# Kernel optimization log

Measured on AMD Instinct MI355X. Metric: run time of the kernel, lower is better.

## Reference

```python
import jax, jax.numpy as jnp
import numpy as np

SLIDING_WINDOW_SIZE = 512  # matches init_kwargs


def setup_inputs() -> dict:
    key = jax.random.key(0)
    kq, kk, kv = jax.random.split(key, 3)
    B, H, L, E = 2, 16, 2048, 128
    q = jax.random.normal(kq, (B, H, L, E), dtype=jnp.float32)
    k = jax.random.normal(kk, (B, H, L, E), dtype=jnp.float32)
    v = jax.random.normal(kv, (B, H, L, E), dtype=jnp.float32)
    return {"q": q, "k": k, "v": v}


def reference(q, k, v):
    # q: (B,H,L,E), k: (B,H,S,E), v: (B,H,S,Ev)
    B, H, L, E = q.shape
    S = k.shape[2]
    scale = jnp.asarray(1.0 / np.sqrt(E), dtype=q.dtype)  # flex_attention default scale
    # Full scores, then score_mod-style masking (faithful to original, which
    # applies -inf after dense score computation without a BlockMask).
    scores = jnp.einsum("bhle,bhse->bhls", q, k) * scale
    q_idx = jnp.arange(L)[:, None]
    k_idx = jnp.arange(S)[None, :]
    # causal: q_idx < k_idx ; window: q_idx - k_idx > window_size
    mask = (q_idx < k_idx) | (q_idx - k_idx > SLIDING_WINDOW_SIZE)
    scores = jnp.where(mask[None, None], -jnp.inf, scores)
    attn = jax.nn.softmax(scores, axis=-1)
    return jnp.einsum("bhls,bhse->bhle", attn, v)
```

## Files before the change

kernel.cpp:

```cpp
#include <hip/hip_runtime.h>


typedef __bf16 bf16_t;
typedef bf16_t bf16x8 __attribute__((ext_vector_type(8)));
typedef float f32x4 __attribute__((ext_vector_type(4)));

union FragU { bf16x8 v; unsigned short s[8]; };

__device__ __forceinline__ unsigned short f2bf(float f) {
    union { float f; unsigned u; } x; x.f = f;
    unsigned u = x.u;
    u += 0x7fffu + ((u >> 16) & 1u);
    return (unsigned short)(u >> 16);
}

constexpr int B_ = 2, H_ = 16, Lq = 2048, E_ = 128, WIN = 512;
constexpr int QT = 64;
constexpr int KT = 32;
constexpr int KSTR = 128;
constexpr int VSTR = 130;
constexpr int PSTR = 40;

#define SCALE_LOG2E 0.1275174364f

extern "C" __global__ __launch_bounds__(256, 2)
void flexattn_kernel(const float* __restrict__ Q,
                     const float* __restrict__ K,
                     const float* __restrict__ V,
                     float* __restrict__ O)
{
    __shared__ unsigned short sK[KT * KSTR];
    __shared__ unsigned short sV[KT * VSTR];
    __shared__ unsigned short sP[4 * 16 * PSTR];

    const int tid  = threadIdx.x;
    const int w    = tid >> 6;
    const int lane = tid & 63;
    const int c    = lane & 15;
    const int g    = lane >> 4;

    const int q0 = blockIdx.x * QT;
    const int bh = blockIdx.y;
    const size_t base = (size_t)bh * Lq * E_;
    const float* Qp = Q + base;
    const float* Kp = K + base;
    const float* Vp = V + base;
    float*       Op = O + base;

    const int qb = q0 + w * 16;

    FragU qf[4];
    {
        const float* qrow = Qp + (size_t)(qb + c) * E_ + g * 8;
        #pragma unroll
        for (int ck = 0; ck < 4; ++ck) {
            #pragma unroll
            for (int j = 0; j < 8; ++j)
                qf[ck].s[j] = f2bf(qrow[ck * 32 + j] * SCALE_LOG2E);
        }
    }

    f32x4 acc[8];
    #pragma unroll
    for (int n = 0; n < 8; ++n) acc[n] = (f32x4){0.f, 0.f, 0.f, 0.f};
    float m_r[4], l_r[4];
    #pragma unroll
    for (int r = 0; r < 4; ++r) { m_r[r] = -1e30f; l_r[r] = 0.f; }

    const int kv_lo = (q0 - WIN) > 0 ? (q0 - WIN) : 0;
    const int kv_hi = q0 + QT;

    for (int kt = kv_lo; kt < kv_hi; kt += KT) {
        __syncthreads();
        #pragma unroll
        for (int i = 0; i < 4; ++i) {
            int fi  = i * 256 + tid;
            int row = fi >> 5;
            int col = (fi & 31) << 2;
            float4 kx = reinterpret_cast<const float4*>(Kp + (size_t)kt * E_)[fi];
            float4 vx = reinterpret_cast<const float4*>(Vp + (size_t)kt * E_)[fi];
            int kcol = col ^ ((row & 7) * 8);
            ushort4 ku;
            ku.x = f2bf(kx.x); ku.y = f2bf(kx.y); ku.z = f2bf(kx.z); ku.w = f2bf(kx.w);
            *reinterpret_cast<ushort4*>(&sK[row * KSTR + kcol]) = ku;
            ushort2 va, vb;
            va.x = f2bf(vx.x); va.y = f2bf(vx.y);
            vb.x = f2bf(vx.z); vb.y = f2bf(vx.w);
            *reinterpret_cast<ushort2*>(&sV[row * VSTR + col])     = va;
            *reinterpret_cast<ushort2*>(&sV[row * VSTR + col + 2]) = vb;
        }
        __syncthreads();

        f32x4 s0 = {0.f,0.f,0.f,0.f}, s1 = {0.f,0.f,0.f,0.f};
        #pragma unroll
        for (int ck = 0; ck < 4; ++ck) {
            int r0 = c;
            int r1 = 16 + c;
            int cb = ck * 32 + g * 8;
            bf16x8 k0 = *reinterpret_cast<const bf16x8*>(&sK[r0 * KSTR + (cb ^ ((r0 & 7) * 8))]);
            bf16x8 k1 = *reinterpret_cast<const bf16x8*>(&sK[r1 * KSTR + (cb ^ ((r1 & 7) * 8))]);
            s0 = __builtin_amdgcn_mfma_f32_16x16x32_bf16(qf[ck].v, k0, s0, 0, 0, 0);
            s1 = __builtin_amdgcn_mfma_f32_16x16x32_bf16(qf[ck].v, k1, s1, 0, 0, 0);
        }

        bool need_mask = (kt + KT - 1 > qb) || ((qb + 15) - kt > WIN);
        if (need_mask) {
            #pragma unroll
            for (int r = 0; r < 4; ++r) {
                int qi  = qb + g * 4 + r;
                int k0i = kt + c;
                int k1i = kt + 16 + c;
                if (k0i > qi || qi - k0i > WIN) s0[r] = -1e30f;
                if (k1i > qi || qi - k1i > WIN) s1[r] = -1e30f;
            }
        }

        #pragma unroll
        for (int r = 0; r < 4; ++r) {
            float t = fmaxf(s0[r], s1[r]);
            #pragma unroll
            for (int off = 1; off < 16; off <<= 1)
                t = fmaxf(t, __shfl_xor(t, off, 16));
            float mnew = fmaxf(m_r[r], t);
            float fac  = exp2f(m_r[r] - mnew);
            float p0   = exp2f(s0[r] - mnew);
            float p1   = exp2f(s1[r] - mnew);
            float rs = p0 + p1;
            #pragma unroll
            for (int off = 1; off < 16; off <<= 1)
                rs += __shfl_xor(rs, off, 16);
            l_r[r] = l_r[r] * fac + rs;
            m_r[r] = mnew;
            #pragma unroll
            for (int n = 0; n < 8; ++n) acc[n][r] *= fac;
            sP[(w * 16 + g * 4 + r) * PSTR + c]      = f2bf(p0);
            sP[(w * 16 + g * 4 + r) * PSTR + 16 + c] = f2bf(p1);
        }

        bf16x8 pa = *reinterpret_cast<const bf16x8*>(&sP[(w * 16 + c) * PSTR + g * 8]);
        #pragma unroll
        for (int n = 0; n < 8; ++n) {
            FragU vf;
            #pragma unroll
            for (int j = 0; j < 8; ++j)
                vf.s[j] = sV[(g * 8 + j) * VSTR + n * 16 + c];
            acc[n] = __builtin_amdgcn_mfma_f32_16x16x32_bf16(pa, vf.v, acc[n], 0, 0, 0);
        }
    }

    #pragma unroll
    for (int r = 0; r < 4; ++r) {
        float inv = 1.0f / l_r[r];
        int qi = qb + g * 4 + r;
        #pragma unroll
        for (int n = 0; n < 8; ++n)
            Op[(size_t)qi * E_ + n * 16 + c] = acc[n][r] * inv;
    }
}

extern "C" void kernel_launch(void* const* d_in, const int* in_sizes, int n_in,
                              void* d_out, int out_size, void* d_ws, size_t ws_size,
                              hipStream_t stream) {
    (void)in_sizes; (void)n_in; (void)out_size; (void)d_ws; (void)ws_size;
    const float* q = (const float*)d_in[0];
    const float* k = (const float*)d_in[1];
    const float* v = (const float*)d_in[2];
    float* o = (float*)d_out;
    dim3 grid(Lq / QT, B_ * H_);
    hipLaunchKernelGGL(flexattn_kernel, grid, dim3(256), 0, stream, q, k, v, o);
}
```

Before: 240.0 us.

## Prefetch next K/V tile into registers, swizzle block order, raise occupancy

Global loads for the next K/V tile are now issued into registers before computing on the current tile, and written to LDS after the compute, so memory latency overlaps the MFMA and softmax work. The grid becomes 1D with a block-index swizzle that spreads consecutive blocks across heads and query tiles, which is meant to balance the uneven per-block work near the sequence start. Launch bounds move from 2 to 4 blocks per SM. The prefetch adds 32 float registers per thread, which works against the tighter register budget that the higher occupancy target imposes and may cause spills.

```diff
diff --git a/kernel.cpp b/kernel.cpp
--- a/kernel.cpp
+++ b/kernel.cpp
@@ -23,7 +23,7 @@
 
 #define SCALE_LOG2E 0.1275174364f
 
-extern "C" __global__ __launch_bounds__(256, 2)
+extern "C" __global__ __launch_bounds__(256, 4)
 void flexattn_kernel(const float* __restrict__ Q,
                      const float* __restrict__ K,
                      const float* __restrict__ V,
@@ -39,8 +39,11 @@
     const int c    = lane & 15;
     const int g    = lane >> 4;
 
-    const int q0 = blockIdx.x * QT;
-    const int bh = blockIdx.y;
+    const int bid = blockIdx.x;
+    const int swz = (bid & 7) * 128 + (bid >> 3);
+    const int q0  = (swz & 31) * QT;
+    const int bh  = swz >> 5;
+
     const size_t base = (size_t)bh * Lq * E_;
     const float* Qp = Q + base;
     const float* Kp = K + base;
@@ -70,26 +73,42 @@
     const int kv_lo = (q0 - WIN) > 0 ? (q0 - WIN) : 0;
     const int kv_hi = q0 + QT;
 
-    for (int kt = kv_lo; kt < kv_hi; kt += KT) {
-        __syncthreads();
+    float4 kr[4], vr[4];
+
+    auto issue_loads = [&](int kt) {
+        const float4* K4 = reinterpret_cast<const float4*>(Kp + (size_t)kt * E_);
+        const float4* V4 = reinterpret_cast<const float4*>(Vp + (size_t)kt * E_);
+        #pragma unroll
+        for (int i = 0; i < 4; ++i) {
+            kr[i] = K4[i * 256 + tid];
+            vr[i] = V4[i * 256 + tid];
+        }
+    };
+    auto write_lds = [&]() {
         #pragma unroll
         for (int i = 0; i < 4; ++i) {
             int fi  = i * 256 + tid;
             int row = fi >> 5;
             int col = (fi & 31) << 2;
-            float4 kx = reinterpret_cast<const float4*>(Kp + (size_t)kt * E_)[fi];
-            float4 vx = reinterpret_cast<const float4*>(Vp + (size_t)kt * E_)[fi];
-            int kcol = col ^ ((row & 7) * 8);
             ushort4 ku;
-            ku.x = f2bf(kx.x); ku.y = f2bf(kx.y); ku.z = f2bf(kx.z); ku.w = f2bf(kx.w);
-            *reinterpret_cast<ushort4*>(&sK[row * KSTR + kcol]) = ku;
-            ushort2 va, vb;
-            va.x = f2bf(vx.x); va.y = f2bf(vx.y);
-            vb.x = f2bf(vx.z); vb.y = f2bf(vx.w);
-            *reinterpret_cast<ushort2*>(&sV[row * VSTR + col])     = va;
-            *reinterpret_cast<ushort2*>(&sV[row * VSTR + col + 2]) = vb;
+            ku.x = f2bf(kr[i].x); ku.y = f2bf(kr[i].y);
+            ku.z = f2bf(kr[i].z); ku.w = f2bf(kr[i].w);
+            *reinterpret_cast<ushort4*>(&sK[row * KSTR + (col ^ ((row & 7) * 8))]) = ku;
+            ushort2 va_, vb_;
+            va_.x = f2bf(vr[i].x); va_.y = f2bf(vr[i].y);
+            vb_.x = f2bf(vr[i].z); vb_.y = f2bf(vr[i].w);
+            *reinterpret_cast<ushort2*>(&sV[row * VSTR + col])     = va_;
+            *reinterpret_cast<ushort2*>(&sV[row * VSTR + col + 2]) = vb_;
         }
-        __syncthreads();
+    };
+
+    issue_loads(kv_lo);
+    write_lds();
+    __syncthreads();
+
+    for (int kt = kv_lo; kt < kv_hi; kt += KT) {
+        const bool more = (kt + KT) < kv_hi;
+        if (more) issue_loads(kt + KT);
 
         f32x4 s0 = {0.f,0.f,0.f,0.f}, s1 = {0.f,0.f,0.f,0.f};
         #pragma unroll
@@ -146,6 +165,10 @@
                 vf.s[j] = sV[(g * 8 + j) * VSTR + n * 16 + c];
             acc[n] = __builtin_amdgcn_mfma_f32_16x16x32_bf16(pa, vf.v, acc[n], 0, 0, 0);
         }
+
+        __syncthreads();
+        if (more) write_lds();
+        __syncthreads();
     }
 
     #pragma unroll
@@ -166,6 +189,6 @@
     const float* k = (const float*)d_in[1];
     const float* v = (const float*)d_in[2];
     float* o = (float*)d_out;
-    dim3 grid(Lq / QT, B_ * H_);
+    dim3 grid((Lq / QT) * (B_ * H_));
     hipLaunchKernelGGL(flexattn_kernel, grid, dim3(256), 0, stream, q, k, v, o);
 }
```

After: 260.4 us. 8.5% more time.
